# Kernel optimization log

Hardware: AMD Instinct MI355X
Metric: run time of the kernel (lower is better)

## Reference

```python
import jax, jax.numpy as jnp
import numpy as np

VOCAB_IN = 32000
VOCAB_OUT = 32000
EMB = 512
HID = 512
BOS = 1
PAD = 0


def lstm_layer(xs, Wih, Whh, b, h0, c0):
    """xs: [T,B,E] -> (ys [T,B,H], hT, cT). PyTorch gate order i,f,g,o."""
    def step(carry, xt):
        h, c = carry
        g = xt @ Wih.T + h @ Whh.T + b
        i, f, gg, o = jnp.split(g, 4, axis=-1)
        c = jax.nn.sigmoid(f) * c + jax.nn.sigmoid(i) * jnp.tanh(gg)
        h = jax.nn.sigmoid(o) * jnp.tanh(c)
        return (h, c), h
    (hT, cT), ys = jax.lax.scan(step, (h0, c0), xs)
    return ys, hT, cT


def setup_inputs() -> dict:
    key = jax.random.key(0)
    ks = jax.random.split(key, 20)
    s = 0.02
    def lstm_params(k, in_dim):
        k1, k2, k3 = jax.random.split(k, 3)
        return (jax.random.normal(k1, (4 * HID, in_dim), jnp.float32) * s,
                jax.random.normal(k2, (4 * HID, HID), jnp.float32) * s,
                jax.random.normal(k3, (4 * HID,), jnp.float32) * s)
    e0_Wih, e0_Whh, e0_b = lstm_params(ks[0], EMB)
    e1_Wih, e1_Whh, e1_b = lstm_params(ks[1], HID)
    d0_Wih, d0_Whh, d0_b = lstm_params(ks[2], EMB)
    d1_Wih, d1_Whh, d1_b = lstm_params(ks[3], HID)
    enc_emb = (jax.random.normal(ks[4], (VOCAB_IN, EMB), jnp.float32) * s).at[PAD].set(0.0)
    dec_emb = (jax.random.normal(ks[5], (VOCAB_OUT, EMB), jnp.float32) * s).at[PAD].set(0.0)
    lin_W = jax.random.normal(ks[6], (VOCAB_OUT, HID), jnp.float32) * s
    lin_b = jax.random.normal(ks[7], (VOCAB_OUT,), jnp.float32) * s
    x = jax.random.randint(ks[8], (32, 64), 0, VOCAB_IN, jnp.int32)
    target_sequence = jax.random.randint(ks[9], (32, 64), 0, VOCAB_OUT, jnp.int32)
    return dict(x=x, target_sequence=target_sequence, enc_emb=enc_emb, dec_emb=dec_emb,
                e0_Wih=e0_Wih, e0_Whh=e0_Whh, e0_b=e0_b,
                e1_Wih=e1_Wih, e1_Whh=e1_Whh, e1_b=e1_b,
                d0_Wih=d0_Wih, d0_Whh=d0_Whh, d0_b=d0_b,
                d1_Wih=d1_Wih, d1_Whh=d1_Whh, d1_b=d1_b,
                lin_W=lin_W, lin_b=lin_b)


def reference(x, target_sequence, enc_emb, dec_emb,
              e0_Wih, e0_Whh, e0_b, e1_Wih, e1_Whh, e1_b,
              d0_Wih, d0_Whh, d0_b, d1_Wih, d1_Whh, d1_b,
              lin_W, lin_b):
    B = x.shape[0]
    z = jnp.zeros((B, HID), enc_emb.dtype)
    # encoder: 2 stacked LSTM layers over source embeddings
    xs = jnp.swapaxes(enc_emb[x], 0, 1)              # [S,B,E]
    y1, h1, c1 = lstm_layer(xs, e0_Wih, e0_Whh, e0_b, z, z)
    _, h2, c2 = lstm_layer(y1, e1_Wih, e1_Whh, e1_b, z, z)
    # decoder: teacher forcing == single scan over BOS-shifted target
    dec_in = jnp.concatenate([jnp.full((B, 1), BOS, target_sequence.dtype),
                              target_sequence[:, :-1]], axis=1)  # [B,T]
    ds = jnp.swapaxes(dec_emb[dec_in], 0, 1)         # [T,B,E]
    u1, _, _ = lstm_layer(ds, d0_Wih, d0_Whh, d0_b, h1, c1)
    u2, _, _ = lstm_layer(u1, d1_Wih, d1_Whh, d1_b, h2, c2)
    logits = u2 @ lin_W.T + lin_b                    # [T,B,V]
    return jnp.swapaxes(logits, 0, 1)                # [B,T,V]
```

## Files before the change

### kernel.cpp

```cpp
#include <hip/hip_runtime.h>


#define BATCH 32
#define T 64
#define HID 512
#define VOCAB 32000
#define BOS 1

typedef unsigned short u16;
typedef unsigned int u32;
typedef __attribute__((ext_vector_type(8))) short bf16x8;
typedef __attribute__((ext_vector_type(4))) float f32x4;

static constexpr size_t MATSZ = (size_t)2048 * 512;

__device__ __forceinline__ float bf2f(u16 u) {
  return __uint_as_float(((u32)u) << 16);
}
__device__ __forceinline__ short f2bfs(float f) {
  u32 x = __float_as_uint(f);
  u32 r = x + 0x7fffu + ((x >> 16) & 1u);
  return (short)(r >> 16);
}

template<bool BF16>
__device__ __forceinline__ bf16x8 ldext8(const void* base, size_t off) {
  if constexpr (BF16) {
    return *(const bf16x8*)((const u16*)base + off);
  } else {
    const float* p = (const float*)base + off;
    float4 a = *(const float4*)p;
    float4 b = *(const float4*)(p + 4);
    bf16x8 r;
    r[0] = f2bfs(a.x); r[1] = f2bfs(a.y); r[2] = f2bfs(a.z); r[3] = f2bfs(a.w);
    r[4] = f2bfs(b.x); r[5] = f2bfs(b.y); r[6] = f2bfs(b.z); r[7] = f2bfs(b.w);
    return r;
  }
}
template<bool BF16>
__device__ __forceinline__ float ldext1(const void* base, size_t off) {
  if constexpr (BF16) return bf2f(((const u16*)base)[off]);
  else return ((const float*)base)[off];
}

__global__ void dtype_probe(const u32* __restrict__ w, int* __restrict__ flag) {
  __shared__ int cnt;
  if (threadIdx.x == 0) cnt = 0;
  __syncthreads();
  int c = 0;
  for (int i = threadIdx.x; i < 1024; i += 256) {
    u16 lo = (u16)(w[i] & 0xFFFFu);
    int e = (lo >> 7) & 0xFF;
    if (e >= 0x68 && e <= 0x7E) c++;
  }
  atomicAdd(&cnt, c);
  __syncthreads();
  if (threadIdx.x == 0) *flag = (cnt > 512) ? 1 : 0;
}

__global__ void init_ws(u16* hz, int* bar) {
  int i = blockIdx.x * 256 + threadIdx.x;
  hz[i] = 0;
  if (i == 0) *bar = 0;
}

struct Ptr8 { const void* p[8]; };

__global__ __launch_bounds__(256) void convert_w(Ptr8 s, u16* __restrict__ dst,
                                                 const int* __restrict__ flag) {
  const int m = blockIdx.z;
  const int i = (blockIdx.x * 256 + threadIdx.x) * 4;
  u16* d = dst + (size_t)m * MATSZ + i;
  if (*flag) {
    *(ushort4*)d = *(const ushort4*)((const u16*)s.p[m] + i);
  } else {
    const float* sp = (const float*)s.p[m] + i;
    float4 v = *(const float4*)sp;
    ushort4 o;
    o.x = (u16)f2bfs(v.x); o.y = (u16)f2bfs(v.y);
    o.z = (u16)f2bfs(v.z); o.w = (u16)f2bfs(v.w);
    *(ushort4*)d = o;
  }
}

__global__ __launch_bounds__(256) void convert_b(Ptr8 s, float* __restrict__ dst,
                                                 const int* __restrict__ flag) {
  const int l = blockIdx.z;
  const int i = blockIdx.x * 256 + threadIdx.x;
  dst[l * 2048 + i] = (*flag) ? bf2f(((const u16*)s.p[l])[i])
                              : ((const float*)s.p[l])[i];
}

template<bool BF16>
__device__ __forceinline__ void gx_body(const int* __restrict__ tokens,
                                        const void* __restrict__ emb,
                                        const u16* __restrict__ wihb,
                                        float* __restrict__ gx, int shift) {
  const int tid = threadIdx.x, lane = tid & 63, w = tid >> 6;
  const int fr = lane & 15, q8 = (lane >> 4) * 8, q4 = (lane >> 4) * 4;
  const int j0 = blockIdx.x * 16;
  const int t = blockIdx.y;
  int t0, t1;
  if (shift) {
    t0 = (t == 0) ? BOS : tokens[fr * T + t - 1];
    t1 = (t == 0) ? BOS : tokens[(fr + 16) * T + t - 1];
  } else {
    t0 = tokens[fr * T + t];
    t1 = tokens[(fr + 16) * T + t];
  }
  const int grow = w * 512 + j0 + fr;
  const u16* wp = wihb + (size_t)grow * 512;
  const size_t e0 = (size_t)t0 * 512, e1 = (size_t)t1 * 512;
  f32x4 acc0 = {0.f, 0.f, 0.f, 0.f}, acc1 = {0.f, 0.f, 0.f, 0.f};
#pragma unroll 4
  for (int ks = 0; ks < 512; ks += 32) {
    bf16x8 b = *(const bf16x8*)(wp + ks + q8);
    bf16x8 a0 = ldext8<BF16>(emb, e0 + ks + q8);
    bf16x8 a1 = ldext8<BF16>(emb, e1 + ks + q8);
    acc0 = __builtin_amdgcn_mfma_f32_16x16x32_bf16(a0, b, acc0, 0, 0, 0);
    acc1 = __builtin_amdgcn_mfma_f32_16x16x32_bf16(a1, b, acc1, 0, 0, 0);
  }
  float* gp = gx + ((size_t)t * 2048 + grow) * 32;
  *(f32x4*)(gp + q4) = acc0;
  *(f32x4*)(gp + 16 + q4) = acc1;
}

__global__ __launch_bounds__(256) void gx_gemm_bf16(
    const int* xtok, const int* dtok, const void* eemb, const void* demb,
    const u16* wbf, float* gxe, float* gxd, const int* __restrict__ flag) {
  if (!*flag) return;
  if (blockIdx.z == 0) gx_body<true>(xtok, eemb, wbf, gxe, 0);
  else                 gx_body<true>(dtok, demb, wbf + 4 * MATSZ, gxd, 1);
}
__global__ __launch_bounds__(256) void gx_gemm_f32(
    const int* xtok, const int* dtok, const void* eemb, const void* demb,
    const u16* wbf, float* gxe, float* gxd, const int* __restrict__ flag) {
  if (*flag) return;
  if (blockIdx.z == 0) gx_body<false>(xtok, eemb, wbf, gxe, 0);
  else                 gx_body<false>(dtok, demb, wbf + 4 * MATSZ, gxd, 1);
}

struct PArgs {
  const u16* wbf;
  const float* biasf;
  const float* gxe;
  const float* gxd;
  const u16* hzero;
  u16* ye0; u16* ye1; u16* yd0; u16* yd1;
  int* bar;
};

__global__ __launch_bounds__(256) void lstm_persist(PArgs A) {
  const int wg = blockIdx.x;
  const bool chB = wg >= 32;
  const int j0 = (wg & 31) * 16;
  const int tid = threadIdx.x;
  const int lane = tid & 63;
  const int w = tid >> 6;
  const int fr = lane & 15;
  const int q8 = (lane >> 4) * 8;
  const int q4 = (lane >> 4) * 4;
  const int NB = BATCH * HID;
  __shared__ float gsh[4][16][33];

  const int bb0 = (tid * 2) & 31,     jj0 = (tid * 2) >> 5;
  const int bb1 = (tid * 2 + 1) & 31, jj1 = (tid * 2 + 1) >> 5;

  bf16x8 wih[16], whh[16];
  float b0i = 0, b0f = 0, b0g = 0, b0o = 0;
  float b1i = 0, b1f = 0, b1g = 0, b1o = 0;
  float c0 = 0.f, c1 = 0.f;
  const int row = w * 512 + j0 + fr;

  for (int k = 0; k < 129; ++k) {
    const int t = chB ? (k - 1) : k;
    if (t >= 0 && t < 128) {
      const int tt = t & 63;
      const bool dec = t >= 64;
      if (tt == 0) {
        const int layer = (dec ? 2 : 0) + (chB ? 1 : 0);
        const u16* whp = A.wbf + (size_t)(2 * layer + 1) * MATSZ + (size_t)row * 512;
#pragma unroll
        for (int kf = 0; kf < 16; ++kf)
          whh[kf] = *(const bf16x8*)(whp + kf * 32 + q8);
        if (chB) {
          const u16* wip = A.wbf + (size_t)(2 * layer) * MATSZ + (size_t)row * 512;
#pragma unroll
          for (int kf = 0; kf < 16; ++kf)
            wih[kf] = *(const bf16x8*)(wip + kf * 32 + q8);
        }
        const float* bp = A.biasf + layer * 2048 + j0;
        b0i = bp[jj0]; b0f = bp[512 + jj0]; b0g = bp[1024 + jj0]; b0o = bp[1536 + jj0];
        b1i = bp[jj1]; b1f = bp[512 + jj1]; b1g = bp[1024 + jj1]; b1o = bp[1536 + jj1];
      }
      const u16 *h_in, *x_in = nullptr;
      u16* y_out;
      const float* gx = nullptr;
      if (!chB) {
        if (!dec) {
          h_in = (tt == 0) ? A.hzero : A.ye0 + (size_t)(tt - 1) * NB;
          y_out = A.ye0 + (size_t)tt * NB;
          gx = A.gxe + (size_t)tt * 2048 * 32;
        } else {
          h_in = (tt == 0) ? A.ye0 + (size_t)63 * NB : A.yd0 + (size_t)(tt - 1) * NB;
          y_out = A.yd0 + (size_t)tt * NB;
          gx = A.gxd + (size_t)tt * 2048 * 32;
        }
      } else {
        if (!dec) {
          x_in = A.ye0 + (size_t)tt * NB;
          h_in = (tt == 0) ? A.hzero : A.ye1 + (size_t)(tt - 1) * NB;
          y_out = A.ye1 + (size_t)tt * NB;
        } else {
          x_in = A.yd0 + (size_t)tt * NB;
          h_in = (tt == 0) ? A.ye1 + (size_t)63 * NB : A.yd1 + (size_t)(tt - 1) * NB;
          y_out = A.yd1 + (size_t)tt * NB;
        }
      }

      f32x4 acc0, acc1;
      if (!chB) {
        const float* gp = gx + (size_t)row * 32;
        acc0 = *(const f32x4*)(gp + q4);
        acc1 = *(const f32x4*)(gp + 16 + q4);
#pragma unroll
        for (int kf = 0; kf < 16; ++kf) {
          bf16x8 h0 = *(const bf16x8*)(h_in + fr * 512 + kf * 32 + q8);
          bf16x8 h1 = *(const bf16x8*)(h_in + (fr + 16) * 512 + kf * 32 + q8);
          acc0 = __builtin_amdgcn_mfma_f32_16x16x32_bf16(h0, whh[kf], acc0, 0, 0, 0);
          acc1 = __builtin_amdgcn_mfma_f32_16x16x32_bf16(h1, whh[kf], acc1, 0, 0, 0);
        }
      } else {
        f32x4 x0a = {0, 0, 0, 0}, x1a = {0, 0, 0, 0};
        f32x4 h0a = {0, 0, 0, 0}, h1a = {0, 0, 0, 0};
#pragma unroll
        for (int kf = 0; kf < 16; ++kf) {
          bf16x8 xa = *(const bf16x8*)(x_in + fr * 512 + kf * 32 + q8);
          bf16x8 xb = *(const bf16x8*)(x_in + (fr + 16) * 512 + kf * 32 + q8);
          bf16x8 ha = *(const bf16x8*)(h_in + fr * 512 + kf * 32 + q8);
          bf16x8 hb = *(const bf16x8*)(h_in + (fr + 16) * 512 + kf * 32 + q8);
          x0a = __builtin_amdgcn_mfma_f32_16x16x32_bf16(xa, wih[kf], x0a, 0, 0, 0);
          x1a = __builtin_amdgcn_mfma_f32_16x16x32_bf16(xb, wih[kf], x1a, 0, 0, 0);
          h0a = __builtin_amdgcn_mfma_f32_16x16x32_bf16(ha, whh[kf], h0a, 0, 0, 0);
          h1a = __builtin_amdgcn_mfma_f32_16x16x32_bf16(hb, whh[kf], h1a, 0, 0, 0);
        }
        acc0 = x0a + h0a;
        acc1 = x1a + h1a;
      }

#pragma unroll
      for (int r = 0; r < 4; ++r) {
        gsh[w][fr][q4 + r] = acc0[r];
        gsh[w][fr][16 + q4 + r] = acc1[r];
      }
      __syncthreads();

      {
        float gi = gsh[0][jj0][bb0] + b0i;
        float gf = gsh[1][jj0][bb0] + b0f;
        float gg = gsh[2][jj0][bb0] + b0g;
        float go = gsh[3][jj0][bb0] + b0o;
        float si = 1.f / (1.f + __expf(-gi));
        float sf = 1.f / (1.f + __expf(-gf));
        float so = 1.f / (1.f + __expf(-go));
        float cn = sf * c0 + si * tanhf(gg);
        c0 = cn;
        y_out[bb0 * 512 + j0 + jj0] = (u16)f2bfs(so * tanhf(cn));

        gi = gsh[0][jj1][bb1] + b1i;
        gf = gsh[1][jj1][bb1] + b1f;
        gg = gsh[2][jj1][bb1] + b1g;
        go = gsh[3][jj1][bb1] + b1o;
        si = 1.f / (1.f + __expf(-gi));
        sf = 1.f / (1.f + __expf(-gf));
        so = 1.f / (1.f + __expf(-go));
        cn = sf * c1 + si * tanhf(gg);
        c1 = cn;
        y_out[bb1 * 512 + j0 + jj1] = (u16)f2bfs(so * tanhf(cn));
      }
    }

    __syncthreads();
    if (tid == 0) {
      __hip_atomic_fetch_add(A.bar, 1, __ATOMIC_RELEASE, __HIP_MEMORY_SCOPE_AGENT);
      const int tgt = 64 * (k + 1);
      while (__hip_atomic_load(A.bar, __ATOMIC_RELAXED, __HIP_MEMORY_SCOPE_AGENT) < tgt)
        __builtin_amdgcn_s_sleep(1);
      __threadfence();
    }
    __syncthreads();
  }
}

template<bool BF16>
__device__ __forceinline__ void out_gemm_body(const u16* __restrict__ A,
                                              const void* __restrict__ Wv,
                                              const void* __restrict__ bias,
                                              void* __restrict__ out) {
  __shared__ __align__(16) u16 As[128 * 40];
  __shared__ __align__(16) u16 Bs[128 * 40];
  const int hw = blockIdx.x;
  const int logical = (hw & 7) * 500 + (hw >> 3);
  const int m0 = (logical & 15) * 128;
  const int n0 = (logical >> 4) * 128;
  const int tid = threadIdx.x;
  const int lane = tid & 63;
  const int wv = tid >> 6;
  const int wm = wv >> 1, wn = wv & 1;
  const int fr = lane & 15, q8 = (lane >> 4) * 8;
  const int r0 = tid >> 2;
  const int c8 = (tid & 3) * 8;

  f32x4 acc[4][4] = {};

  for (int k0 = 0; k0 < 512; k0 += 32) {
    __syncthreads();
    *(uint4*)&As[r0 * 40 + c8]        = *(const uint4*)&A[(size_t)(m0 + r0) * 512 + k0 + c8];
    *(uint4*)&As[(r0 + 64) * 40 + c8] = *(const uint4*)&A[(size_t)(m0 + r0 + 64) * 512 + k0 + c8];
    *(bf16x8*)&Bs[r0 * 40 + c8]        = ldext8<BF16>(Wv, (size_t)(n0 + r0) * 512 + k0 + c8);
    *(bf16x8*)&Bs[(r0 + 64) * 40 + c8] = ldext8<BF16>(Wv, (size_t)(n0 + r0 + 64) * 512 + k0 + c8);
    __syncthreads();
    bf16x8 af[4], bg[4];
#pragma unroll
    for (int i = 0; i < 4; ++i) {
      af[i] = *(const bf16x8*)&As[(wm * 64 + i * 16 + fr) * 40 + q8];
      bg[i] = *(const bf16x8*)&Bs[(wn * 64 + i * 16 + fr) * 40 + q8];
    }
#pragma unroll
    for (int i = 0; i < 4; ++i)
#pragma unroll
      for (int j = 0; j < 4; ++j)
        acc[i][j] = __builtin_amdgcn_mfma_f32_16x16x32_bf16(af[i], bg[j], acc[i][j], 0, 0, 0);
  }

  const int cl = lane & 15;
  const int rq = (lane >> 4) * 4;
#pragma unroll
  for (int j = 0; j < 4; ++j) {
    int n = n0 + wn * 64 + j * 16 + cl;
    float bv = ldext1<BF16>(bias, n);
#pragma unroll
    for (int i = 0; i < 4; ++i) {
#pragma unroll
      for (int r = 0; r < 4; ++r) {
        int m = m0 + wm * 64 + i * 16 + rq + r;
        int tt = m >> 5, bb = m & 31;
        size_t oidx = ((size_t)bb * T + tt) * VOCAB + n;
        float v = acc[i][j][r] + bv;
        if constexpr (BF16) __builtin_nontemporal_store((u16)f2bfs(v), (u16*)out + oidx);
        else                __builtin_nontemporal_store(v, (float*)out + oidx);
      }
    }
  }
}

__global__ __launch_bounds__(256) void out_gemm_bf16(const u16* A, const void* Wv,
                                                     const void* bias, void* out,
                                                     const int* __restrict__ flag) {
  if (!*flag) return;
  out_gemm_body<true>(A, Wv, bias, out);
}
__global__ __launch_bounds__(256) void out_gemm_f32(const u16* A, const void* Wv,
                                                    const void* bias, void* out,
                                                    const int* __restrict__ flag) {
  if (*flag) return;
  out_gemm_body<false>(A, Wv, bias, out);
}

extern "C" void kernel_launch(void* const* d_in, const int* in_sizes, int n_in,
                              void* d_out, int out_size, void* d_ws, size_t ws_size,
                              hipStream_t stream) {
  (void)in_sizes; (void)n_in; (void)out_size; (void)ws_size;
  const int* x = (const int*)d_in[0];
  const int* tgt = (const int*)d_in[1];
  const void* enc_emb = d_in[2];
  const void* dec_emb = d_in[3];
  const void* Wih[4] = {d_in[4], d_in[7], d_in[10], d_in[13]};
  const void* Whh[4] = {d_in[5], d_in[8], d_in[11], d_in[14]};
  const void* bias[4] = {d_in[6], d_in[9], d_in[12], d_in[15]};
  const void* lin_W = d_in[16];
  const void* lin_b = d_in[17];

  char* ws = (char*)d_ws;
  u16* y_e0   = (u16*)(ws + 0x000000);
  u16* y_e1   = (u16*)(ws + 0x200000);
  u16* y_d0   = (u16*)(ws + 0x400000);
  u16* y_d1   = (u16*)(ws + 0x600000);
  u16* h_zero = (u16*)(ws + 0x800000);
  int* flag   = (int*)(ws + 0x810000);
  int* bar    = (int*)(ws + 0x810100);
  float* biasf = (float*)(ws + 0x820000);
  u16* wbf    = (u16*)(ws + 0x830000);
  float* gxe  = (float*)(ws + 0x1830000);
  float* gxd  = (float*)(ws + 0x2830000);

  dtype_probe<<<dim3(1), 256, 0, stream>>>((const u32*)lin_W, flag);
  init_ws<<<dim3(64), 256, 0, stream>>>(h_zero, bar);

  Ptr8 wsrc;
  for (int l = 0; l < 4; ++l) { wsrc.p[2 * l] = Wih[l]; wsrc.p[2 * l + 1] = Whh[l]; }
  convert_w<<<dim3(1024, 1, 8), 256, 0, stream>>>(wsrc, wbf, flag);

  Ptr8 bsrc = {};
  for (int l = 0; l < 4; ++l) bsrc.p[l] = bias[l];
  convert_b<<<dim3(8, 1, 4), 256, 0, stream>>>(bsrc, biasf, flag);

  gx_gemm_bf16<<<dim3(32, 64, 2), 256, 0, stream>>>(x, tgt, enc_emb, dec_emb, wbf, gxe, gxd, flag);
  gx_gemm_f32 <<<dim3(32, 64, 2), 256, 0, stream>>>(x, tgt, enc_emb, dec_emb, wbf, gxe, gxd, flag);

  PArgs pa;
  pa.wbf = wbf; pa.biasf = biasf; pa.gxe = gxe; pa.gxd = gxd;
  pa.hzero = h_zero;
  pa.ye0 = y_e0; pa.ye1 = y_e1; pa.yd0 = y_d0; pa.yd1 = y_d1;
  pa.bar = bar;
  lstm_persist<<<dim3(64), 256, 0, stream>>>(pa);

  out_gemm_bf16<<<dim3(4000), 256, 0, stream>>>(y_d1, lin_W, lin_b, d_out, flag);
  out_gemm_f32 <<<dim3(4000), 256, 0, stream>>>(y_d1, lin_W, lin_b, d_out, flag);
}
```

Baseline: 2.316 ms.

## Fuse both LSTM layers into each workgroup with LDS-staged inputs and split barrier

The persistent LSTM kernel now runs on 32 workgroups instead of 64. Each workgroup computes both the layer-0 and layer-1 stages for its 16 hidden units in a wavefront-pipelined schedule, sharing the layer-0 output tile as the input to both. Shared x/h tiles are staged once into LDS per step rather than each wave reading them from global memory. The grid barrier is split so the arrive happens early, overlapping the gx prefetch and weight loads with the wait, and outputs are written with relaxed packed 32-bit atomic stores. Each workgroup now holds three weight fragments in registers and does more MFMA work per step, trading per-step compute for fewer barrier participants and less global traffic.

```diff
diff --git a/kernel.cpp b/kernel.cpp
--- a/kernel.cpp
+++ b/kernel.cpp
@@ -6,6 +6,7 @@
 #define HID 512
 #define VOCAB 32000
 #define BOS 1
+#define NB (BATCH * HID)
 
 typedef unsigned short u16;
 typedef unsigned int u32;
@@ -150,143 +151,191 @@
   int* bar;
 };
 
-__global__ __launch_bounds__(256) void lstm_persist(PArgs A) {
+__global__ __launch_bounds__(256, 1) void lstm_persist(PArgs A) {
   const int wg = blockIdx.x;
-  const bool chB = wg >= 32;
-  const int j0 = (wg & 31) * 16;
+  const int j0 = wg * 16;
   const int tid = threadIdx.x;
   const int lane = tid & 63;
   const int w = tid >> 6;
   const int fr = lane & 15;
   const int q8 = (lane >> 4) * 8;
   const int q4 = (lane >> 4) * 4;
-  const int NB = BATCH * HID;
-  __shared__ float gsh[4][16][33];
-
-  const int bb0 = (tid * 2) & 31,     jj0 = (tid * 2) >> 5;
-  const int bb1 = (tid * 2 + 1) & 31, jj1 = (tid * 2 + 1) >> 5;
-
-  bf16x8 wih[16], whh[16];
-  float b0i = 0, b0f = 0, b0g = 0, b0o = 0;
-  float b1i = 0, b1f = 0, b1g = 0, b1o = 0;
-  float c0 = 0.f, c1 = 0.f;
-  const int row = w * 512 + j0 + fr;
-
-  for (int k = 0; k < 129; ++k) {
-    const int t = chB ? (k - 1) : k;
-    if (t >= 0 && t < 128) {
-      const int tt = t & 63;
-      const bool dec = t >= 64;
-      if (tt == 0) {
-        const int layer = (dec ? 2 : 0) + (chB ? 1 : 0);
-        const u16* whp = A.wbf + (size_t)(2 * layer + 1) * MATSZ + (size_t)row * 512;
-#pragma unroll
-        for (int kf = 0; kf < 16; ++kf)
-          whh[kf] = *(const bf16x8*)(whp + kf * 32 + q8);
-        if (chB) {
-          const u16* wip = A.wbf + (size_t)(2 * layer) * MATSZ + (size_t)row * 512;
-#pragma unroll
-          for (int kf = 0; kf < 16; ++kf)
-            wih[kf] = *(const bf16x8*)(wip + kf * 32 + q8);
-        }
-        const float* bp = A.biasf + layer * 2048 + j0;
-        b0i = bp[jj0]; b0f = bp[512 + jj0]; b0g = bp[1024 + jj0]; b0o = bp[1536 + jj0];
-        b1i = bp[jj1]; b1f = bp[512 + jj1]; b1g = bp[1024 + jj1]; b1o = bp[1536 + jj1];
-      }
-      const u16 *h_in, *x_in = nullptr;
-      u16* y_out;
-      const float* gx = nullptr;
-      if (!chB) {
-        if (!dec) {
-          h_in = (tt == 0) ? A.hzero : A.ye0 + (size_t)(tt - 1) * NB;
-          y_out = A.ye0 + (size_t)tt * NB;
-          gx = A.gxe + (size_t)tt * 2048 * 32;
-        } else {
-          h_in = (tt == 0) ? A.ye0 + (size_t)63 * NB : A.yd0 + (size_t)(tt - 1) * NB;
-          y_out = A.yd0 + (size_t)tt * NB;
-          gx = A.gxd + (size_t)tt * 2048 * 32;
-        }
-      } else {
-        if (!dec) {
-          x_in = A.ye0 + (size_t)tt * NB;
-          h_in = (tt == 0) ? A.hzero : A.ye1 + (size_t)(tt - 1) * NB;
-          y_out = A.ye1 + (size_t)tt * NB;
-        } else {
-          x_in = A.yd0 + (size_t)tt * NB;
-          h_in = (tt == 0) ? A.ye1 + (size_t)63 * NB : A.yd1 + (size_t)(tt - 1) * NB;
-          y_out = A.yd1 + (size_t)tt * NB;
-        }
-      }
-
-      f32x4 acc0, acc1;
-      if (!chB) {
-        const float* gp = gx + (size_t)row * 32;
-        acc0 = *(const f32x4*)(gp + q4);
-        acc1 = *(const f32x4*)(gp + 16 + q4);
-#pragma unroll
-        for (int kf = 0; kf < 16; ++kf) {
-          bf16x8 h0 = *(const bf16x8*)(h_in + fr * 512 + kf * 32 + q8);
-          bf16x8 h1 = *(const bf16x8*)(h_in + (fr + 16) * 512 + kf * 32 + q8);
-          acc0 = __builtin_amdgcn_mfma_f32_16x16x32_bf16(h0, whh[kf], acc0, 0, 0, 0);
-          acc1 = __builtin_amdgcn_mfma_f32_16x16x32_bf16(h1, whh[kf], acc1, 0, 0, 0);
-        }
-      } else {
-        f32x4 x0a = {0, 0, 0, 0}, x1a = {0, 0, 0, 0};
-        f32x4 h0a = {0, 0, 0, 0}, h1a = {0, 0, 0, 0};
-#pragma unroll
-        for (int kf = 0; kf < 16; ++kf) {
-          bf16x8 xa = *(const bf16x8*)(x_in + fr * 512 + kf * 32 + q8);
-          bf16x8 xb = *(const bf16x8*)(x_in + (fr + 16) * 512 + kf * 32 + q8);
-          bf16x8 ha = *(const bf16x8*)(h_in + fr * 512 + kf * 32 + q8);
-          bf16x8 hb = *(const bf16x8*)(h_in + (fr + 16) * 512 + kf * 32 + q8);
-          x0a = __builtin_amdgcn_mfma_f32_16x16x32_bf16(xa, wih[kf], x0a, 0, 0, 0);
-          x1a = __builtin_amdgcn_mfma_f32_16x16x32_bf16(xb, wih[kf], x1a, 0, 0, 0);
-          h0a = __builtin_amdgcn_mfma_f32_16x16x32_bf16(ha, whh[kf], h0a, 0, 0, 0);
-          h1a = __builtin_amdgcn_mfma_f32_16x16x32_bf16(hb, whh[kf], h1a, 0, 0, 0);
-        }
-        acc0 = x0a + h0a;
-        acc1 = x1a + h1a;
-      }
-
-#pragma unroll
-      for (int r = 0; r < 4; ++r) {
-        gsh[w][fr][q4 + r] = acc0[r];
-        gsh[w][fr][16 + q4 + r] = acc1[r];
-      }
-      __syncthreads();
-
-      {
-        float gi = gsh[0][jj0][bb0] + b0i;
-        float gf = gsh[1][jj0][bb0] + b0f;
-        float gg = gsh[2][jj0][bb0] + b0g;
-        float go = gsh[3][jj0][bb0] + b0o;
-        float si = 1.f / (1.f + __expf(-gi));
-        float sf = 1.f / (1.f + __expf(-gf));
-        float so = 1.f / (1.f + __expf(-go));
-        float cn = sf * c0 + si * tanhf(gg);
-        c0 = cn;
-        y_out[bb0 * 512 + j0 + jj0] = (u16)f2bfs(so * tanhf(cn));
-
-        gi = gsh[0][jj1][bb1] + b1i;
-        gf = gsh[1][jj1][bb1] + b1f;
-        gg = gsh[2][jj1][bb1] + b1g;
-        go = gsh[3][jj1][bb1] + b1o;
-        si = 1.f / (1.f + __expf(-gi));
-        sf = 1.f / (1.f + __expf(-gf));
-        so = 1.f / (1.f + __expf(-go));
-        cn = sf * c1 + si * tanhf(gg);
-        c1 = cn;
-        y_out[bb1 * 512 + j0 + jj1] = (u16)f2bfs(so * tanhf(cn));
-      }
-    }
-
-    __syncthreads();
-    if (tid == 0) {
-      __hip_atomic_fetch_add(A.bar, 1, __ATOMIC_RELEASE, __HIP_MEMORY_SCOPE_AGENT);
-      const int tgt = 64 * (k + 1);
+  const int row = w * HID + j0 + fr;
+
+  __shared__ __align__(16) u16 SX[32 * 520];
+  __shared__ __align__(16) u16 SH[32 * 520];
+  __shared__ float gshA[4][16][33];
+  __shared__ float gshB[4][16][33];
+
+  bf16x8 whhA[16], wihB[16], whhB[16];
+  float bA[8], bB[8];
+  float cA0 = 0.f, cA1 = 0.f, cB0 = 0.f, cB1 = 0.f;
+
+  const int jj0 = (2 * tid) & 15;
+  const int bb = tid >> 3;
+
+  auto loadW = [&](bf16x8* dst, int mat) {
+    const u16* p = A.wbf + (size_t)mat * MATSZ + (size_t)row * HID + q8;
+#pragma unroll
+    for (int kf = 0; kf < 16; ++kf) dst[kf] = *(const bf16x8*)(p + kf * 32);
+  };
+  auto loadB = [&](float* d, int layer) {
+    const float* bp = A.biasf + layer * 2048 + j0;
+    d[0] = bp[jj0];        d[1] = bp[jj0 + 1];
+    d[2] = bp[512 + jj0];  d[3] = bp[512 + jj0 + 1];
+    d[4] = bp[1024 + jj0]; d[5] = bp[1024 + jj0 + 1];
+    d[6] = bp[1536 + jj0]; d[7] = bp[1536 + jj0 + 1];
+  };
+
+  for (int k = 0; k <= 128; ++k) {
+    const bool aAct = k < 128;
+    const bool bAct = k >= 1;
+
+    if (bAct && tid == 0)
+      __hip_atomic_fetch_add(A.bar, 1, __ATOMIC_RELAXED, __HIP_MEMORY_SCOPE_AGENT);
+
+    f32x4 gxp0 = {0.f, 0.f, 0.f, 0.f}, gxp1 = {0.f, 0.f, 0.f, 0.f};
+    if (aAct) {
+      const float* gp = ((k < 64) ? A.gxe + (size_t)k * 65536
+                                  : A.gxd + (size_t)(k - 64) * 65536)
+                        + (size_t)row * 32;
+      gxp0 = *(const f32x4*)(gp + q4);
+      gxp1 = *(const f32x4*)(gp + 16 + q4);
+    }
+    if (k == 0)  { loadW(whhA, 1); loadW(wihB, 2); loadW(whhB, 3);
+                   loadB(bA, 0); loadB(bB, 1); }
+    if (k == 64) { loadW(whhA, 5); loadB(bA, 2); }
+    if (k == 65) { loadW(wihB, 6); loadW(whhB, 7); loadB(bB, 3); }
+
+    if (bAct && tid == 0) {
+      const int tgt = 32 * k;
       while (__hip_atomic_load(A.bar, __ATOMIC_RELAXED, __HIP_MEMORY_SCOPE_AGENT) < tgt)
         __builtin_amdgcn_s_sleep(1);
-      __threadfence();
+    }
+    __syncthreads();
+
+    const u16* srcX = (k == 0)  ? A.hzero
+                    : (k <= 64) ? A.ye0 + (size_t)(k - 1) * NB
+                                : A.yd0 + (size_t)(k - 65) * NB;
+    const u16* srcH = (k <= 1)  ? A.hzero
+                    : (k <= 65) ? A.ye1 + (size_t)(k - 2) * NB
+                                : A.yd1 + (size_t)(k - 66) * NB;
+    {
+      uint4 tx[8], th[8];
+#pragma unroll
+      for (int i = 0; i < 8; ++i) {
+        const int q = i * 256 + tid, r = q >> 6, c = q & 63;
+        tx[i] = *(const uint4*)(srcX + r * 512 + c * 8);
+      }
+      if (bAct) {
+#pragma unroll
+        for (int i = 0; i < 8; ++i) {
+          const int q = i * 256 + tid, r = q >> 6, c = q & 63;
+          th[i] = *(const uint4*)(srcH + r * 512 + c * 8);
+        }
+      }
+#pragma unroll
+      for (int i = 0; i < 8; ++i) {
+        const int q = i * 256 + tid, r = q >> 6, c = q & 63;
+        *(uint4*)&SX[r * 520 + c * 8] = tx[i];
+      }
+      if (bAct) {
+#pragma unroll
+        for (int i = 0; i < 8; ++i) {
+          const int q = i * 256 + tid, r = q >> 6, c = q & 63;
+          *(uint4*)&SH[r * 520 + c * 8] = th[i];
+        }
+      }
+    }
+    __syncthreads();
+
+    const int rx0 = fr * 520 + q8, rx1 = (fr + 16) * 520 + q8;
+    f32x4 accA0 = gxp0, accA1 = gxp1;
+    f32x4 xb0 = {0,0,0,0}, xb1 = {0,0,0,0}, hb0 = {0,0,0,0}, hb1 = {0,0,0,0};
+    if (aAct && bAct) {
+#pragma unroll
+      for (int kf = 0; kf < 16; ++kf) {
+        bf16x8 a0 = *(const bf16x8*)&SX[rx0 + kf * 32];
+        bf16x8 a1 = *(const bf16x8*)&SX[rx1 + kf * 32];
+        bf16x8 h0 = *(const bf16x8*)&SH[rx0 + kf * 32];
+        bf16x8 h1 = *(const bf16x8*)&SH[rx1 + kf * 32];
+        accA0 = __builtin_amdgcn_mfma_f32_16x16x32_bf16(a0, whhA[kf], accA0, 0, 0, 0);
+        accA1 = __builtin_amdgcn_mfma_f32_16x16x32_bf16(a1, whhA[kf], accA1, 0, 0, 0);
+        xb0 = __builtin_amdgcn_mfma_f32_16x16x32_bf16(a0, wihB[kf], xb0, 0, 0, 0);
+        xb1 = __builtin_amdgcn_mfma_f32_16x16x32_bf16(a1, wihB[kf], xb1, 0, 0, 0);
+        hb0 = __builtin_amdgcn_mfma_f32_16x16x32_bf16(h0, whhB[kf], hb0, 0, 0, 0);
+        hb1 = __builtin_amdgcn_mfma_f32_16x16x32_bf16(h1, whhB[kf], hb1, 0, 0, 0);
+      }
+    } else if (aAct) {
+#pragma unroll
+      for (int kf = 0; kf < 16; ++kf) {
+        bf16x8 a0 = *(const bf16x8*)&SX[rx0 + kf * 32];
+        bf16x8 a1 = *(const bf16x8*)&SX[rx1 + kf * 32];
+        accA0 = __builtin_amdgcn_mfma_f32_16x16x32_bf16(a0, whhA[kf], accA0, 0, 0, 0);
+        accA1 = __builtin_amdgcn_mfma_f32_16x16x32_bf16(a1, whhA[kf], accA1, 0, 0, 0);
+      }
+    } else {
+#pragma unroll
+      for (int kf = 0; kf < 16; ++kf) {
+        bf16x8 a0 = *(const bf16x8*)&SX[rx0 + kf * 32];
+        bf16x8 a1 = *(const bf16x8*)&SX[rx1 + kf * 32];
+        bf16x8 h0 = *(const bf16x8*)&SH[rx0 + kf * 32];
+        bf16x8 h1 = *(const bf16x8*)&SH[rx1 + kf * 32];
+        xb0 = __builtin_amdgcn_mfma_f32_16x16x32_bf16(a0, wihB[kf], xb0, 0, 0, 0);
+        xb1 = __builtin_amdgcn_mfma_f32_16x16x32_bf16(a1, wihB[kf], xb1, 0, 0, 0);
+        hb0 = __builtin_amdgcn_mfma_f32_16x16x32_bf16(h0, whhB[kf], hb0, 0, 0, 0);
+        hb1 = __builtin_amdgcn_mfma_f32_16x16x32_bf16(h1, whhB[kf], hb1, 0, 0, 0);
+      }
+    }
+
+    if (aAct) {
+#pragma unroll
+      for (int r = 0; r < 4; ++r) {
+        gshA[w][fr][q4 + r] = accA0[r];
+        gshA[w][fr][16 + q4 + r] = accA1[r];
+      }
+    }
+    if (bAct) {
+      f32x4 sb0 = xb0 + hb0, sb1 = xb1 + hb1;
+#pragma unroll
+      for (int r = 0; r < 4; ++r) {
+        gshB[w][fr][q4 + r] = sb0[r];
+        gshB[w][fr][16 + q4 + r] = sb1[r];
+      }
+    }
+    __syncthreads();
+
+    if (aAct) {
+      u16* yA = (k < 64) ? A.ye0 + (size_t)k * NB : A.yd0 + (size_t)(k - 64) * NB;
+      float gi0 = gshA[0][jj0][bb] + bA[0], gi1 = gshA[0][jj0 + 1][bb] + bA[1];
+      float gf0 = gshA[1][jj0][bb] + bA[2], gf1 = gshA[1][jj0 + 1][bb] + bA[3];
+      float gg0 = gshA[2][jj0][bb] + bA[4], gg1 = gshA[2][jj0 + 1][bb] + bA[5];
+      float go0 = gshA[3][jj0][bb] + bA[6], go1 = gshA[3][jj0 + 1][bb] + bA[7];
+      float cn0 = (1.f / (1.f + __expf(-gf0))) * cA0
+                + (1.f / (1.f + __expf(-gi0))) * tanhf(gg0);
+      float cn1 = (1.f / (1.f + __expf(-gf1))) * cA1
+                + (1.f / (1.f + __expf(-gi1))) * tanhf(gg1);
+      cA0 = cn0; cA1 = cn1;
+      u32 y0 = (u16)f2bfs((1.f / (1.f + __expf(-go0))) * tanhf(cn0));
+      u32 y1 = (u16)f2bfs((1.f / (1.f + __expf(-go1))) * tanhf(cn1));
+      __hip_atomic_store((u32*)(yA + bb * 512 + j0 + jj0), y0 | (y1 << 16),
+                         __ATOMIC_RELAXED, __HIP_MEMORY_SCOPE_AGENT);
+    }
+    if (bAct) {
+      u16* yB = (k <= 64) ? A.ye1 + (size_t)(k - 1) * NB : A.yd1 + (size_t)(k - 65) * NB;
+      float gi0 = gshB[0][jj0][bb] + bB[0], gi1 = gshB[0][jj0 + 1][bb] + bB[1];
+      float gf0 = gshB[1][jj0][bb] + bB[2], gf1 = gshB[1][jj0 + 1][bb] + bB[3];
+      float gg0 = gshB[2][jj0][bb] + bB[4], gg1 = gshB[2][jj0 + 1][bb] + bB[5];
+      float go0 = gshB[3][jj0][bb] + bB[6], go1 = gshB[3][jj0 + 1][bb] + bB[7];
+      float cn0 = (1.f / (1.f + __expf(-gf0))) * cB0
+                + (1.f / (1.f + __expf(-gi0))) * tanhf(gg0);
+      float cn1 = (1.f / (1.f + __expf(-gf1))) * cB1
+                + (1.f / (1.f + __expf(-gi1))) * tanhf(gg1);
+      cB0 = cn0; cB1 = cn1;
+      u32 y0 = (u16)f2bfs((1.f / (1.f + __expf(-go0))) * tanhf(cn0));
+      u32 y1 = (u16)f2bfs((1.f / (1.f + __expf(-go1))) * tanhf(cn1));
+      __hip_atomic_store((u32*)(yB + bb * 512 + j0 + jj0), y0 | (y1 << 16),
+                         __ATOMIC_RELAXED, __HIP_MEMORY_SCOPE_AGENT);
     }
     __syncthreads();
   }
@@ -413,7 +462,7 @@
   pa.hzero = h_zero;
   pa.ye0 = y_e0; pa.ye1 = y_e1; pa.yd0 = y_d0; pa.yd1 = y_d1;
   pa.bar = bar;
-  lstm_persist<<<dim3(64), 256, 0, stream>>>(pa);
+  lstm_persist<<<dim3(32), 256, 0, stream>>>(pa);
 
   out_gemm_bf16<<<dim3(4000), 256, 0, stream>>>(y_d1, lin_W, lin_b, d_out, flag);
   out_gemm_f32 <<<dim3(4000), 256, 0, stream>>>(y_d1, lin_W, lin_b, d_out, flag);
```

Measured after the change: 1.893 ms. 18.3% less time.
